# Kernel tuning notes

Hardware: AMD Instinct MI355X
Metric: run time of the kernel (lower is better)

The kernel has to match this reference:

```python
import jax, jax.numpy as jnp
import numpy as np

B, S, C = 8192, 7, 30


def _iou(b1, b2):
    """Faithful replica of calculate_iou (including its intersect/area1 + area2 - intersect quirk).
    b1, b2: [..., 4] as (cx, cy, w, h). Returns [...] ."""
    area1 = b1[..., 2] * b1[..., 3]
    area2 = b2[..., 2] * b2[..., 3]
    max_left = jnp.maximum(b1[..., 0] - b1[..., 2] / 2, b2[..., 0] - b2[..., 2] / 2)
    min_right = jnp.minimum(b1[..., 0] + b1[..., 2] / 2, b2[..., 0] + b2[..., 2] / 2)
    max_top = jnp.maximum(b1[..., 1] - b1[..., 3] / 2, b2[..., 1] - b2[..., 3] / 2)
    min_bottom = jnp.minimum(b1[..., 1] + b1[..., 3] / 2, b2[..., 1] + b2[..., 3] / 2)
    inter = (min_right - max_left) * (min_bottom - max_top)
    overlap = (max_left < min_right) & (max_top < min_bottom)
    return jnp.where(overlap, inter / area1 + area2 - inter, 0.0)


def setup_inputs() -> dict:
    key = jax.random.key(0)
    k1, k2, k3 = jax.random.split(key, 3)
    preds = jax.random.uniform(k1, (B, S, S, C), dtype=jnp.float32, minval=0.01, maxval=1.0)
    labels = jax.random.uniform(k2, (B, S, S, C), dtype=jnp.float32, minval=0.01, maxval=1.0)
    obj = (jax.random.uniform(k3, (B, S, S)) < 0.3).astype(jnp.float32)
    labels = labels.at[..., 4].set(obj)  # objectness indicator in {0,1}
    return {"preds": preds, "labels": labels}


def reference(preds, labels):
    batch_size = labels.shape[0]
    obj = (labels[..., 4] == 1).astype(preds.dtype)  # [B,7,7]

    # IoUs are computed on detached values in the original (numpy round-trip)
    iou1 = jax.lax.stop_gradient(_iou(preds[..., 0:4], labels[..., 0:4]))
    iou2 = jax.lax.stop_gradient(_iou(preds[..., 5:9], labels[..., 5:9]))
    resp1 = iou1 > iou2  # box 1 responsible

    xy1 = jnp.sum((preds[..., 0:2] - labels[..., 0:2]) ** 2, axis=-1)
    xy2 = jnp.sum((preds[..., 5:7] - labels[..., 5:7]) ** 2, axis=-1)
    wh1 = jnp.sum((jnp.sqrt(preds[..., 2:4]) - jnp.sqrt(labels[..., 2:4])) ** 2, axis=-1)
    wh2 = jnp.sum((jnp.sqrt(preds[..., 7:9]) - jnp.sqrt(labels[..., 7:9])) ** 2, axis=-1)

    loss_xy = 5.0 * jnp.where(resp1, xy1, xy2)
    loss_wh = jnp.where(resp1, wh1, wh2)
    loss_obj = jnp.where(resp1, (preds[..., 4] - iou1) ** 2, (preds[..., 9] - iou2) ** 2)
    loss_noobj_objcell = 0.5 * jnp.where(resp1, (preds[..., 9] - iou2) ** 2, (preds[..., 4] - iou1) ** 2)
    loss_cls = jnp.sum((preds[..., 10:] - labels[..., 10:]) ** 2, axis=-1)

    obj_cell = loss_xy + loss_wh + loss_obj + loss_noobj_objcell + loss_cls
    noobj_cell = 0.5 * (preds[..., 4] ** 2 + preds[..., 9] ** 2)

    total = jnp.sum(obj * obj_cell + (1.0 - obj) * noobj_cell)
    return total / batch_size
```

## Files before the change

### kernel.cpp

```cpp
#include <hip/hip_runtime.h>

#define YB     8192
#define YS     7
#define YC     30
#define NCELLS (YB * YS * YS)
#define CPT    128
#define NBLK   (NCELLS / CPT)
#define BLOCK  256

__device__ __forceinline__ float iou_quirk(float cx1, float cy1, float w1, float h1,
                                           float cx2, float cy2, float w2, float h2) {
    float area1 = w1 * h1;
    float area2 = w2 * h2;
    float max_left   = fmaxf(cx1 - w1 * 0.5f, cx2 - w2 * 0.5f);
    float min_right  = fminf(cx1 + w1 * 0.5f, cx2 + w2 * 0.5f);
    float max_top    = fmaxf(cy1 - h1 * 0.5f, cy2 - h2 * 0.5f);
    float min_bottom = fminf(cy1 + h1 * 0.5f, cy2 + h2 * 0.5f);
    float inter = (min_right - max_left) * (min_bottom - max_top);
    bool overlap = (max_left < min_right) && (max_top < min_bottom);
    return overlap ? (inter / area1 + area2 - inter) : 0.0f;
}

__global__ __launch_bounds__(BLOCK) void yolo_partial_kernel(const float* __restrict__ preds,
                                                             const float* __restrict__ labels,
                                                             float* __restrict__ partial) {
    __shared__ float sp[CPT * YC];
    __shared__ float sl[CPT * YC];
    __shared__ float wsum[2];

    const int tid = threadIdx.x;
    const long base = (long)blockIdx.x * (CPT * YC);

    const float4* gp = (const float4*)(preds + base);
    const float4* gl = (const float4*)(labels + base);
    float4* sp4 = (float4*)sp;
    float4* sl4 = (float4*)sl;
    const int NV = CPT * YC / 4;

#if defined(__has_builtin) && __has_builtin(__builtin_amdgcn_global_load_lds)
    typedef const __attribute__((address_space(1))) void* as1_t;
    typedef __attribute__((address_space(3))) void* as3_t;
    for (int i = tid; i < NV; i += BLOCK)
        __builtin_amdgcn_global_load_lds((as1_t)(gp + i), (as3_t)(sp4 + i), 16, 0, 0);
    for (int i = tid; i < NV; i += BLOCK)
        __builtin_amdgcn_global_load_lds((as1_t)(gl + i), (as3_t)(sl4 + i), 16, 0, 0);
#else
    for (int i = tid; i < NV; i += BLOCK) {
        sp4[i] = gp[i];
        sl4[i] = gl[i];
    }
#endif
    __syncthreads();

    float v = 0.0f;
    if (tid < CPT) {
        const float2* p2 = (const float2*)(sp + tid * YC);
        const float2* l2 = (const float2*)(sl + tid * YC);
        float pv[YC], lv[YC];
        #pragma unroll
        for (int i = 0; i < YC / 2; ++i) {
            float2 a = p2[i]; pv[2 * i] = a.x; pv[2 * i + 1] = a.y;
            float2 b = l2[i]; lv[2 * i] = b.x; lv[2 * i + 1] = b.y;
        }

        float iou1 = iou_quirk(pv[0], pv[1], pv[2], pv[3], lv[0], lv[1], lv[2], lv[3]);
        float iou2 = iou_quirk(pv[5], pv[6], pv[7], pv[8], lv[5], lv[6], lv[7], lv[8]);
        bool resp1 = iou1 > iou2;

        float dx1 = pv[0] - lv[0], dy1 = pv[1] - lv[1];
        float xy1 = dx1 * dx1 + dy1 * dy1;
        float dx2 = pv[5] - lv[5], dy2 = pv[6] - lv[6];
        float xy2 = dx2 * dx2 + dy2 * dy2;

        float sw1 = sqrtf(pv[2]) - sqrtf(lv[2]), sh1 = sqrtf(pv[3]) - sqrtf(lv[3]);
        float wh1 = sw1 * sw1 + sh1 * sh1;
        float sw2 = sqrtf(pv[7]) - sqrtf(lv[7]), sh2 = sqrtf(pv[8]) - sqrtf(lv[8]);
        float wh2 = sw2 * sw2 + sh2 * sh2;

        float d1 = pv[4] - iou1, d2 = pv[9] - iou2;
        float e1 = d1 * d1, e2 = d2 * d2;

        float loss_xy = 5.0f * (resp1 ? xy1 : xy2);
        float loss_wh = resp1 ? wh1 : wh2;
        float loss_obj = resp1 ? e1 : e2;
        float loss_noobj_objcell = 0.5f * (resp1 ? e2 : e1);

        float loss_cls = 0.0f;
        #pragma unroll
        for (int c = 10; c < YC; ++c) {
            float d = pv[c] - lv[c];
            loss_cls += d * d;
        }

        float obj_cell = loss_xy + loss_wh + loss_obj + loss_noobj_objcell + loss_cls;
        float noobj_cell = 0.5f * (pv[4] * pv[4] + pv[9] * pv[9]);

        v = (lv[4] == 1.0f) ? obj_cell : noobj_cell;
    }

    if (tid < CPT) {
        for (int off = 32; off > 0; off >>= 1) v += __shfl_down(v, off);
        if ((tid & 63) == 0) wsum[tid >> 6] = v;
    }
    __syncthreads();
    if (tid == 0) partial[blockIdx.x] = wsum[0] + wsum[1];
}

__global__ __launch_bounds__(BLOCK) void yolo_final_kernel(const float* __restrict__ partial,
                                                           float* __restrict__ out) {
    __shared__ double w[BLOCK / 64];
    double s = 0.0;
    for (int i = threadIdx.x; i < NBLK; i += BLOCK) s += (double)partial[i];
    for (int off = 32; off > 0; off >>= 1) s += __shfl_down(s, off);
    const int lane = threadIdx.x & 63, wid = threadIdx.x >> 6;
    if (lane == 0) w[wid] = s;
    __syncthreads();
    if (threadIdx.x == 0) out[0] = (float)((w[0] + w[1] + w[2] + w[3]) / (double)YB);
}

extern "C" void kernel_launch(void* const* d_in, const int* in_sizes, int n_in,
                              void* d_out, int out_size, void* d_ws, size_t ws_size,
                              hipStream_t stream) {
    const float* preds  = (const float*)d_in[0];
    const float* labels = (const float*)d_in[1];
    float* out = (float*)d_out;
    float* partial = (float*)d_ws;

    yolo_partial_kernel<<<NBLK, BLOCK, 0, stream>>>(preds, labels, partial);
    yolo_final_kernel<<<1, BLOCK, 0, stream>>>(partial, out);
}
```

Baseline: 25.18 us.

## Fuse partial and final reduction kernels with last-block atomic and direct loads

Replaces the two-kernel reduction with a single kernel where the last block, detected by an atomic counter, sums all partials. It also drops LDS staging so each of the 256 threads loads its own cell directly from global memory with float2 reads. The aim is to remove a kernel launch and the idle half-block. The cost is an added memset launch, and per-thread strided loads that are less coalesced than the previous cooperative staging.

```diff
diff --git a/kernel.cpp b/kernel.cpp
--- a/kernel.cpp
+++ b/kernel.cpp
@@ -4,9 +4,8 @@
 #define YS     7
 #define YC     30
 #define NCELLS (YB * YS * YS)
-#define CPT    128
-#define NBLK   (NCELLS / CPT)
 #define BLOCK  256
+#define NBLK   (NCELLS / BLOCK)
 
 __device__ __forceinline__ float iou_quirk(float cx1, float cy1, float w1, float h1,
                                            float cx2, float cy2, float w2, float h2) {
@@ -21,101 +20,84 @@
     return overlap ? (inter / area1 + area2 - inter) : 0.0f;
 }
 
-__global__ __launch_bounds__(BLOCK) void yolo_partial_kernel(const float* __restrict__ preds,
-                                                             const float* __restrict__ labels,
-                                                             float* __restrict__ partial) {
-    __shared__ float sp[CPT * YC];
-    __shared__ float sl[CPT * YC];
-    __shared__ float wsum[2];
+__global__ __launch_bounds__(BLOCK) void yolo_fused_kernel(const float* __restrict__ preds,
+                                                           const float* __restrict__ labels,
+                                                           float* __restrict__ partial,
+                                                           unsigned int* __restrict__ counter,
+                                                           float* __restrict__ out) {
+    const int tid = threadIdx.x;
+    const long cell = (long)blockIdx.x * BLOCK + tid;
 
-    const int tid = threadIdx.x;
-    const long base = (long)blockIdx.x * (CPT * YC);
+    const float2* p2 = (const float2*)(preds + cell * YC);
+    const float2* l2 = (const float2*)(labels + cell * YC);
 
-    const float4* gp = (const float4*)(preds + base);
-    const float4* gl = (const float4*)(labels + base);
-    float4* sp4 = (float4*)sp;
-    float4* sl4 = (float4*)sl;
-    const int NV = CPT * YC / 4;
+    float pv[10], lv[10];
+    #pragma unroll
+    for (int i = 0; i < 5; ++i) {
+        float2 a = p2[i]; pv[2 * i] = a.x; pv[2 * i + 1] = a.y;
+        float2 b = l2[i]; lv[2 * i] = b.x; lv[2 * i + 1] = b.y;
+    }
+    float loss_cls = 0.0f;
+    #pragma unroll
+    for (int i = 5; i < 15; ++i) {
+        float2 a = p2[i], b = l2[i];
+        float dx = a.x - b.x, dy = a.y - b.y;
+        loss_cls += dx * dx + dy * dy;
+    }
 
-#if defined(__has_builtin) && __has_builtin(__builtin_amdgcn_global_load_lds)
-    typedef const __attribute__((address_space(1))) void* as1_t;
-    typedef __attribute__((address_space(3))) void* as3_t;
-    for (int i = tid; i < NV; i += BLOCK)
-        __builtin_amdgcn_global_load_lds((as1_t)(gp + i), (as3_t)(sp4 + i), 16, 0, 0);
-    for (int i = tid; i < NV; i += BLOCK)
-        __builtin_amdgcn_global_load_lds((as1_t)(gl + i), (as3_t)(sl4 + i), 16, 0, 0);
-#else
-    for (int i = tid; i < NV; i += BLOCK) {
-        sp4[i] = gp[i];
-        sl4[i] = gl[i];
-    }
-#endif
+    float iou1 = iou_quirk(pv[0], pv[1], pv[2], pv[3], lv[0], lv[1], lv[2], lv[3]);
+    float iou2 = iou_quirk(pv[5], pv[6], pv[7], pv[8], lv[5], lv[6], lv[7], lv[8]);
+    bool resp1 = iou1 > iou2;
+
+    float dx1 = pv[0] - lv[0], dy1 = pv[1] - lv[1];
+    float xy1 = dx1 * dx1 + dy1 * dy1;
+    float dx2 = pv[5] - lv[5], dy2 = pv[6] - lv[6];
+    float xy2 = dx2 * dx2 + dy2 * dy2;
+
+    float sw1 = sqrtf(pv[2]) - sqrtf(lv[2]), sh1 = sqrtf(pv[3]) - sqrtf(lv[3]);
+    float wh1 = sw1 * sw1 + sh1 * sh1;
+    float sw2 = sqrtf(pv[7]) - sqrtf(lv[7]), sh2 = sqrtf(pv[8]) - sqrtf(lv[8]);
+    float wh2 = sw2 * sw2 + sh2 * sh2;
+
+    float d1 = pv[4] - iou1, d2 = pv[9] - iou2;
+    float e1 = d1 * d1, e2 = d2 * d2;
+
+    float loss_xy = 5.0f * (resp1 ? xy1 : xy2);
+    float loss_wh = resp1 ? wh1 : wh2;
+    float loss_obj = resp1 ? e1 : e2;
+    float loss_noobj_objcell = 0.5f * (resp1 ? e2 : e1);
+
+    float obj_cell = loss_xy + loss_wh + loss_obj + loss_noobj_objcell + loss_cls;
+    float noobj_cell = 0.5f * (pv[4] * pv[4] + pv[9] * pv[9]);
+
+    float v = (lv[4] == 1.0f) ? obj_cell : noobj_cell;
+
+    __shared__ float wsum[BLOCK / 64];
+    __shared__ int is_last;
+    for (int off = 32; off > 0; off >>= 1) v += __shfl_down(v, off);
+    const int lane = tid & 63, wid = tid >> 6;
+    if (lane == 0) wsum[wid] = v;
     __syncthreads();
 
-    float v = 0.0f;
-    if (tid < CPT) {
-        const float2* p2 = (const float2*)(sp + tid * YC);
-        const float2* l2 = (const float2*)(sl + tid * YC);
-        float pv[YC], lv[YC];
-        #pragma unroll
-        for (int i = 0; i < YC / 2; ++i) {
-            float2 a = p2[i]; pv[2 * i] = a.x; pv[2 * i + 1] = a.y;
-            float2 b = l2[i]; lv[2 * i] = b.x; lv[2 * i + 1] = b.y;
-        }
-
-        float iou1 = iou_quirk(pv[0], pv[1], pv[2], pv[3], lv[0], lv[1], lv[2], lv[3]);
-        float iou2 = iou_quirk(pv[5], pv[6], pv[7], pv[8], lv[5], lv[6], lv[7], lv[8]);
-        bool resp1 = iou1 > iou2;
-
-        float dx1 = pv[0] - lv[0], dy1 = pv[1] - lv[1];
-        float xy1 = dx1 * dx1 + dy1 * dy1;
-        float dx2 = pv[5] - lv[5], dy2 = pv[6] - lv[6];
-        float xy2 = dx2 * dx2 + dy2 * dy2;
-
-        float sw1 = sqrtf(pv[2]) - sqrtf(lv[2]), sh1 = sqrtf(pv[3]) - sqrtf(lv[3]);
-        float wh1 = sw1 * sw1 + sh1 * sh1;
-        float sw2 = sqrtf(pv[7]) - sqrtf(lv[7]), sh2 = sqrtf(pv[8]) - sqrtf(lv[8]);
-        float wh2 = sw2 * sw2 + sh2 * sh2;
-
-        float d1 = pv[4] - iou1, d2 = pv[9] - iou2;
-        float e1 = d1 * d1, e2 = d2 * d2;
-
-        float loss_xy = 5.0f * (resp1 ? xy1 : xy2);
-        float loss_wh = resp1 ? wh1 : wh2;
-        float loss_obj = resp1 ? e1 : e2;
-        float loss_noobj_objcell = 0.5f * (resp1 ? e2 : e1);
-
-        float loss_cls = 0.0f;
-        #pragma unroll
-        for (int c = 10; c < YC; ++c) {
-            float d = pv[c] - lv[c];
-            loss_cls += d * d;
-        }
-
-        float obj_cell = loss_xy + loss_wh + loss_obj + loss_noobj_objcell + loss_cls;
-        float noobj_cell = 0.5f * (pv[4] * pv[4] + pv[9] * pv[9]);
-
-        v = (lv[4] == 1.0f) ? obj_cell : noobj_cell;
-    }
-
-    if (tid < CPT) {
-        for (int off = 32; off > 0; off >>= 1) v += __shfl_down(v, off);
-        if ((tid & 63) == 0) wsum[tid >> 6] = v;
+    if (tid == 0) {
+        partial[blockIdx.x] = wsum[0] + wsum[1] + wsum[2] + wsum[3];
+        __threadfence();
+        unsigned int prev = atomicAdd(counter, 1u);
+        is_last = (prev == (unsigned int)(NBLK - 1));
     }
     __syncthreads();
-    if (tid == 0) partial[blockIdx.x] = wsum[0] + wsum[1];
-}
 
-__global__ __launch_bounds__(BLOCK) void yolo_final_kernel(const float* __restrict__ partial,
-                                                           float* __restrict__ out) {
-    __shared__ double w[BLOCK / 64];
-    double s = 0.0;
-    for (int i = threadIdx.x; i < NBLK; i += BLOCK) s += (double)partial[i];
-    for (int off = 32; off > 0; off >>= 1) s += __shfl_down(s, off);
-    const int lane = threadIdx.x & 63, wid = threadIdx.x >> 6;
-    if (lane == 0) w[wid] = s;
-    __syncthreads();
-    if (threadIdx.x == 0) out[0] = (float)((w[0] + w[1] + w[2] + w[3]) / (double)YB);
+    if (is_last) {
+        __threadfence();
+        const volatile float* vp = (const volatile float*)partial;
+        double s = 0.0;
+        for (int i = tid; i < NBLK; i += BLOCK) s += (double)vp[i];
+        for (int off = 32; off > 0; off >>= 1) s += __shfl_down(s, off);
+        __shared__ double w[BLOCK / 64];
+        if (lane == 0) w[wid] = s;
+        __syncthreads();
+        if (tid == 0) out[0] = (float)((w[0] + w[1] + w[2] + w[3]) / (double)YB);
+    }
 }
 
 extern "C" void kernel_launch(void* const* d_in, const int* in_sizes, int n_in,
@@ -125,7 +107,8 @@
     const float* labels = (const float*)d_in[1];
     float* out = (float*)d_out;
     float* partial = (float*)d_ws;
+    unsigned int* counter = (unsigned int*)((char*)d_ws + 6272);
 
-    yolo_partial_kernel<<<NBLK, BLOCK, 0, stream>>>(preds, labels, partial);
-    yolo_final_kernel<<<1, BLOCK, 0, stream>>>(partial, out);
+    hipMemsetAsync(counter, 0, sizeof(unsigned int), stream);
+    yolo_fused_kernel<<<NBLK, BLOCK, 0, stream>>>(preds, labels, partial, counter, out);
 }
```

Result: slower. 73.88 us (+193.4%).
